# Performance work log

Hardware: AMD Instinct MI355X
Metric: run time of the kernel (lower is better)

## Reference

```python
import jax, jax.numpy as jnp
import numpy as np

B, N, DIM, NL, E = 8, 4096, 128, 3, 524288
NN = B * N


def setup_inputs() -> dict:
    key = jax.random.key(0)
    kx, ke, kw = jax.random.split(key, 3)
    x = jax.random.normal(kx, (B, N, DIM), dtype=jnp.float32)
    batch_edge_index = jax.random.randint(ke, (2, E), 0, NN, dtype=jnp.int32)
    wks = jax.random.split(kw, NL)
    Ws = jnp.stack([jax.random.normal(k, (DIM, DIM), dtype=jnp.float32) / np.sqrt(DIM)
                    for k in wks])  # [NL, DIM, DIM]
    bs = jnp.zeros((NL, DIM), dtype=jnp.float32)
    return {"x": x, "batch_edge_index": batch_edge_index, "Ws": Ws, "bs": bs}


def _gcn_layer(x, W, b, row, col, deg_inv_sqrt, n):
    # PyG GCNConv: h = x @ W; symmetric normalization over edges+self-loops;
    # scatter-add messages at targets (col); add bias.
    h = x @ W  # [n, DIM]
    norm = deg_inv_sqrt[row] * deg_inv_sqrt[col]  # [E+n]
    msg = h[row] * norm[:, None]  # gather at sources, scale
    return jax.ops.segment_sum(msg, col, num_segments=n) + b


def reference(x, batch_edge_index, Ws, bs):
    nb, npts, d = x.shape
    n = nb * npts
    h = x.reshape(n, d)
    # add self-loops once (same edge structure for all layers)
    loops = jnp.arange(n, dtype=batch_edge_index.dtype)
    row = jnp.concatenate([batch_edge_index[0], loops])
    col = jnp.concatenate([batch_edge_index[1], loops])
    deg = jax.ops.segment_sum(jnp.ones_like(col, dtype=h.dtype), col, num_segments=n)
    deg_inv_sqrt = jnp.where(deg > 0, jax.lax.rsqrt(jnp.maximum(deg, 1e-12)), 0.0)
    for i in range(NL):
        out = _gcn_layer(h, Ws[i], bs[i], row, col, deg_inv_sqrt, n)
        h = jax.nn.relu(h + out)  # residual + relu (dropout = identity in eval)
    return h.reshape(nb, npts, d)
```

## Files before the change

### kernel.cpp

```cpp
#include <hip/hip_runtime.h>


typedef __attribute__((ext_vector_type(8))) short short8;
typedef __attribute__((ext_vector_type(4))) float f32x4;
typedef __attribute__((ext_vector_type(2))) float f32x2;

__device__ inline ushort f2bf(float f) {
    union { float f; unsigned u; } v; v.f = f;
    unsigned u = v.u;
    return (ushort)((u + 0x7fffu + ((u >> 16) & 1u)) >> 16);
}
__device__ inline float2 bf2f(unsigned u) {
    union { unsigned i; float f; } a, b;
    a.i = u << 16;
    b.i = u & 0xffff0000u;
    return make_float2(a.f, b.f);
}
__device__ inline short8 pack8(f32x4 a, f32x4 b) {
    short8 r = { (short)f2bf(a.x), (short)f2bf(a.y), (short)f2bf(a.z), (short)f2bf(a.w),
                 (short)f2bf(b.x), (short)f2bf(b.y), (short)f2bf(b.z), (short)f2bf(b.w) };
    return r;
}
__device__ inline unsigned char f2fp8(float f) {
    return (unsigned char)(__builtin_amdgcn_cvt_pk_fp8_f32(f, f, 0, false) & 0xff);
}
__device__ inline float2 fp8x2(ushort v) {
    f32x2 lo = __builtin_amdgcn_cvt_pk_f32_fp8((int)v, false);
    return make_float2(lo.x, lo.y);
}

__global__ __launch_bounds__(256) void k_scan1(const int* __restrict__ deg,
                                               int* __restrict__ offs,
                                               int* __restrict__ bsum, int n) {
    __shared__ int sm[256];
    int t = threadIdx.x, i = blockIdx.x * 256 + t;
    int v = (i < n) ? deg[i] : 0;
    sm[t] = v;
    __syncthreads();
    for (int off = 1; off < 256; off <<= 1) {
        int u = (t >= off) ? sm[t - off] : 0;
        __syncthreads();
        sm[t] += u;
        __syncthreads();
    }
    if (i < n) offs[i] = sm[t] - v;
    if (t == 255) bsum[blockIdx.x] = sm[255];
}

__global__ __launch_bounds__(256) void k_scan3(int* __restrict__ offs,
                                               const int* __restrict__ bsum,
                                               const int* __restrict__ deg,
                                               int* __restrict__ cnt,
                                               float* __restrict__ dis,
                                               unsigned* __restrict__ g32,
                                               int n, int E) {
    __shared__ int red[256];
    int t = threadIdx.x, bid = blockIdx.x;
    red[t] = (t < 128 && t < bid) ? bsum[t] : 0;
    __syncthreads();
    for (int off = 128; off >= 1; off >>= 1) {
        if (t < off) red[t] += red[t + off];
        __syncthreads();
    }
    int base = red[0];
    int i = bid * 256 + t;
    if (i < n) {
        int o = offs[i] + base;
        offs[i] = o;
        cnt[i] = o;
        dis[i] = rsqrtf((float)(deg[i] + 1));
    }
    if (i == 0) offs[n] = E;
    if (i < 32) g32[(size_t)n * 32 + i] = 0;
}

__global__ void k_csr(const int* __restrict__ row, const int* __restrict__ col,
                      int* __restrict__ cnt, ushort* __restrict__ csru, int E) {
    int i = blockIdx.x * blockDim.x + threadIdx.x;
    if (i < E) {
        int c = col[i];
        int p = atomicAdd(&cnt[c], 1);
        csru[p] = (ushort)row[i];
    }
}

#define GEMM_BODY(A0, A1, A2, A3)                                               \
    f32x4 acc[8] = {};                                                          \
    _Pragma("unroll")                                                           \
    for (int nf = 0; nf < 8; ++nf) {                                            \
        const unsigned* wr = &Wl[nf * 16 + c][0];                               \
        int sx = (c & 7) << 2;                                                  \
        int b = q * 4;                                                          \
        short8 b0 = *(const short8*)(wr + ((b +  0) ^ sx));                     \
        short8 b1 = *(const short8*)(wr + ((b + 16) ^ sx));                     \
        short8 b2 = *(const short8*)(wr + ((b + 32) ^ sx));                     \
        short8 b3 = *(const short8*)(wr + ((b + 48) ^ sx));                     \
        acc[nf] = __builtin_amdgcn_mfma_f32_16x16x32_bf16(A0, b0, acc[nf], 0, 0, 0); \
        acc[nf] = __builtin_amdgcn_mfma_f32_16x16x32_bf16(A1, b1, acc[nf], 0, 0, 0); \
        acc[nf] = __builtin_amdgcn_mfma_f32_16x16x32_bf16(A2, b2, acc[nf], 0, 0, 0); \
        acc[nf] = __builtin_amdgcn_mfma_f32_16x16x32_bf16(A3, b3, acc[nf], 0, 0, 0); \
    }                                                                           \
    _Pragma("unroll")                                                           \
    for (int nf = 0; nf < 8; ++nf) {                                            \
        int gc = nf * 16 + c;                                                   \
        g[(size_t)(rb + q * 4 + 0) * 128 + gc] = f2fp8(acc[nf][0]);             \
        g[(size_t)(rb + q * 4 + 1) * 128 + gc] = f2fp8(acc[nf][1]);             \
        g[(size_t)(rb + q * 4 + 2) * 128 + gc] = f2fp8(acc[nf][2]);             \
        g[(size_t)(rb + q * 4 + 3) * 128 + gc] = f2fp8(acc[nf][3]);             \
    }

#define W_STAGE(TILE)                                                            \
    __shared__ unsigned Wl[128][64];                                             \
    int tid = threadIdx.x;                                                       \
    {                                                                            \
        int nn = tid & 127, hf = tid >> 7;                                       \
        for (int qq = 0; qq < 32; ++qq) {                                        \
            int k2 = hf * 32 + qq;                                               \
            float lo = W[(size_t)(2 * k2) * 128 + nn];                           \
            float hi = W[(size_t)(2 * k2 + 1) * 128 + nn];                       \
            Wl[nn][k2 ^ ((nn & 7) << 2)] = ((unsigned)f2bf(hi) << 16) | f2bf(lo);\
        }                                                                        \
    }                                                                            \
    __syncthreads();                                                             \
    int w = tid >> 6, l = tid & 63;                                              \
    int rb = (TILE) * 64 + w * 16;                                               \
    int c = l & 15, q = l >> 4;

__global__ __launch_bounds__(256) void k_gemm(const unsigned* __restrict__ hb,
                                              const float* __restrict__ W,
                                              unsigned char* __restrict__ g, int n) {
    W_STAGE(blockIdx.x)
    const short8* arow = (const short8*)(hb + (size_t)(rb + c) * 64);
    short8 a0 = arow[q], a1 = arow[4 + q], a2 = arow[8 + q], a3 = arow[12 + q];
    GEMM_BODY(a0, a1, a2, a3)
}

__global__ __launch_bounds__(256) void k_l0(const float* __restrict__ x,
                                            const float* __restrict__ W,
                                            unsigned char* __restrict__ g,
                                            const int* __restrict__ col,
                                            int* __restrict__ deg,
                                            int n, int E) {
    int gtiles = n >> 6;
    if ((int)blockIdx.x >= gtiles) {
        int i = ((int)blockIdx.x - gtiles) * 256 + threadIdx.x;
        if (i < E) atomicAdd(&deg[col[i]], 1);
        return;
    }
    W_STAGE((int)blockIdx.x)
    const f32x4* xr = (const f32x4*)(x + (size_t)(rb + c) * 128);
    short8 a0 = pack8(xr[q * 2 +  0], xr[q * 2 +  1]);
    short8 a1 = pack8(xr[q * 2 +  8], xr[q * 2 +  9]);
    short8 a2 = pack8(xr[q * 2 + 16], xr[q * 2 + 17]);
    short8 a3 = pack8(xr[q * 2 + 24], xr[q * 2 + 25]);
    GEMM_BODY(a0, a1, a2, a3)
}

__global__ __launch_bounds__(256) void k_gather(const ushort* __restrict__ g,
                                                unsigned* __restrict__ hb,
                                                const float* __restrict__ dis,
                                                const float* __restrict__ bias,
                                                const int* __restrict__ offs,
                                                const ushort* __restrict__ csru,
                                                const float* __restrict__ xres,
                                                float* __restrict__ outp,
                                                int n, int use_x, int last) {
    int wid = threadIdx.x >> 6, lane = threadIdx.x & 63;
    int node = blockIdx.x * 4 + wid;
    if (node >= n) return;

    float dn = dis[node];
    float2 acc;
    {
        float2 f = fp8x2(g[(size_t)node * 64 + lane]);
        acc.x = f.x * dn; acc.y = f.y * dn;
    }
    int s = offs[node];
    int deg = offs[node + 1] - s;
    for (int j0 = 0; j0 < deg; j0 += 64) {
        int rem = deg - j0;
        int m = rem < 64 ? rem : 64;
        int idx = n; float dsl = 0.f;
        if (lane < m) {
            idx = (int)__builtin_nontemporal_load(&csru[s + j0 + lane]);
            dsl = dis[idx];
        }
        int mc = (m + 15) & ~15;
        for (int t = 0; t < mc; t += 16) {
            ushort v[16];
#pragma unroll
            for (int u = 0; u < 16; ++u) {
                int r = __shfl(idx, t + u, 64);
                v[u] = g[(size_t)r * 64 + lane];
            }
            float ds[16];
#pragma unroll
            for (int u = 0; u < 16; ++u) ds[u] = __shfl(dsl, t + u, 64);
#pragma unroll
            for (int u = 0; u < 16; ++u) {
                float2 f = fp8x2(v[u]);
                acc.x = fmaf(f.x, ds[u], acc.x);
                acc.y = fmaf(f.y, ds[u], acc.y);
            }
        }
    }

    float2 bv = ((const float2*)bias)[lane];
    float2 hv;
    if (use_x) {
        hv = ((const float2*)xres)[(size_t)node * 64 + lane];
    } else {
        hv = bf2f(hb[(size_t)node * 64 + lane]);
    }
    float ox = fmaxf(hv.x + acc.x * dn + bv.x, 0.f);
    float oy = fmaxf(hv.y + acc.y * dn + bv.y, 0.f);
    if (last) {
        f32x2 o = { ox, oy };
        __builtin_nontemporal_store(o, (f32x2*)&outp[(size_t)node * 128 + lane * 2]);
    } else {
        hb[(size_t)node * 64 + lane] = ((unsigned)f2bf(oy) << 16) | f2bf(ox);
    }
}

static inline size_t al256(size_t x) { return (x + 255) & ~(size_t)255; }

extern "C" void kernel_launch(void* const* d_in, const int* in_sizes, int n_in,
                              void* d_out, int out_size, void* d_ws, size_t ws_size,
                              hipStream_t stream) {
    const float* x  = (const float*)d_in[0];
    const int*   ei = (const int*)d_in[1];
    const float* Ws = (const float*)d_in[2];
    const float* bs = (const float*)d_in[3];
    int n  = in_sizes[0] / 128;
    int E  = in_sizes[1] / 2;
    int NL = in_sizes[2] / (128 * 128);
    const int* rowp = ei;
    const int* colp = ei + E;

    char* ws = (char*)d_ws;
    size_t gplane  = al256((size_t)(n + 1) * 128);
    size_t hplane  = al256((size_t)(n + 1) * 256);
    unsigned char* g  = (unsigned char*)ws;
    unsigned*      hb = (unsigned*)(ws + gplane);
    char* p = ws + gplane + hplane;
    float* dis  = (float*)p;               p += al256((size_t)n * 4);
    int*   deg  = (int*)p;                 p += al256((size_t)n * 4);
    int*   offs = (int*)p;                 p += al256((size_t)(n + 1) * 4);
    int*   cnt  = (int*)p;                 p += al256((size_t)n * 4);
    int*   bsum = (int*)p;                 p += 512;
    ushort* csru = (ushort*)p;

    int nb = (n + 255) / 256;
    int gtiles = n / 64;
    int eblocks = (E + 255) / 256;

    (void)hipMemsetAsync(deg, 0, (size_t)n * 4, stream);
    k_l0<<<gtiles + eblocks, 256, 0, stream>>>(x, Ws, g, colp, deg, n, E);
    k_scan1<<<nb, 256, 0, stream>>>(deg, offs, bsum, n);
    k_scan3<<<nb, 256, 0, stream>>>(offs, bsum, deg, cnt, dis, (unsigned*)g, n, E);
    k_csr<<<eblocks, 256, 0, stream>>>(rowp, colp, cnt, csru, E);

    for (int l = 0; l < NL; ++l) {
        int last = (l + 1 == NL);
        if (l > 0)
            k_gemm<<<gtiles, 256, 0, stream>>>(hb, Ws + (size_t)l * 128 * 128,
                                               g, n);
        k_gather<<<(n + 3) / 4, 256, 0, stream>>>((const ushort*)g, hb, dis,
                                                  bs + (size_t)l * 128,
                                                  offs, csru, x,
                                                  (float*)d_out, n,
                                                  l == 0, last);
    }
}
```

Before: 150.3 us.

## Prescale GEMM output by source norm and gather two nodes per wavefront

Moves the per-source degree normalization out of the gather and into the producer: the GEMM epilogue multiplies each row by dis before the fp8 store, and k_scan3 rescales layer-0 rows in place. The gather then needs no per-edge dis lookup or shuffle and reduces to pure fp8 sums. Each half-wave handles one node with 4-byte loads (4 fp8 values per lane), so one wavefront covers two nodes. Tree-style partial sums replace the serial FMAs. The trade-off is an extra fp8 quantization after scaling, plus an extra read-modify-write pass over g in k_scan3.

```diff
diff --git a/kernel.cpp b/kernel.cpp
--- a/kernel.cpp
+++ b/kernel.cpp
@@ -4,6 +4,7 @@
 typedef __attribute__((ext_vector_type(8))) short short8;
 typedef __attribute__((ext_vector_type(4))) float f32x4;
 typedef __attribute__((ext_vector_type(2))) float f32x2;
+typedef __attribute__((ext_vector_type(2))) unsigned u32x2;
 
 __device__ inline ushort f2bf(float f) {
     union { float f; unsigned u; } v; v.f = f;
@@ -16,6 +17,11 @@
     b.i = u & 0xffff0000u;
     return make_float2(a.f, b.f);
 }
+__device__ inline f32x4 bf4(u32x2 v) {
+    float2 a = bf2f(v.x), b = bf2f(v.y);
+    f32x4 r = { a.x, a.y, b.x, b.y };
+    return r;
+}
 __device__ inline short8 pack8(f32x4 a, f32x4 b) {
     short8 r = { (short)f2bf(a.x), (short)f2bf(a.y), (short)f2bf(a.z), (short)f2bf(a.w),
                  (short)f2bf(b.x), (short)f2bf(b.y), (short)f2bf(b.z), (short)f2bf(b.w) };
@@ -24,9 +30,16 @@
 __device__ inline unsigned char f2fp8(float f) {
     return (unsigned char)(__builtin_amdgcn_cvt_pk_fp8_f32(f, f, 0, false) & 0xff);
 }
-__device__ inline float2 fp8x2(ushort v) {
+__device__ inline unsigned pack4fp8(f32x4 v) {
+    unsigned u = (unsigned)__builtin_amdgcn_cvt_pk_fp8_f32(v.x, v.y, 0, false);
+    u = (unsigned)__builtin_amdgcn_cvt_pk_fp8_f32(v.z, v.w, (int)u, true);
+    return u;
+}
+__device__ inline f32x4 fp8x4(unsigned v) {
     f32x2 lo = __builtin_amdgcn_cvt_pk_f32_fp8((int)v, false);
-    return make_float2(lo.x, lo.y);
+    f32x2 hi = __builtin_amdgcn_cvt_pk_f32_fp8((int)v, true);
+    f32x4 r = { lo.x, lo.y, hi.x, hi.y };
+    return r;
 }
 
 __global__ __launch_bounds__(256) void k_scan1(const int* __restrict__ deg,
@@ -64,14 +77,28 @@
     }
     int base = red[0];
     int i = bid * 256 + t;
+    float dv = 0.f;
     if (i < n) {
         int o = offs[i] + base;
         offs[i] = o;
         cnt[i] = o;
-        dis[i] = rsqrtf((float)(deg[i] + 1));
+        dv = rsqrtf((float)(deg[i] + 1));
+        dis[i] = dv;
     }
     if (i == 0) offs[n] = E;
     if (i < 32) g32[(size_t)n * 32 + i] = 0;
+
+    int lane = t & 63;
+    int wbase = bid * 256 + (t & ~63);
+    int hl = lane & 31, sel = lane >> 5;
+    for (int rr = 0; rr < 64; rr += 2) {
+        int row = wbase + rr + sel;
+        float d = __shfl(dv, rr + sel, 64);
+        if (row < n) {
+            unsigned u = g32[(size_t)row * 32 + hl];
+            g32[(size_t)row * 32 + hl] = pack4fp8(fp8x4(u) * d);
+        }
+    }
 }
 
 __global__ void k_csr(const int* __restrict__ row, const int* __restrict__ col,
@@ -84,7 +111,7 @@
     }
 }
 
-#define GEMM_BODY(A0, A1, A2, A3)                                               \
+#define GEMM_MAIN(A0, A1, A2, A3)                                               \
     f32x4 acc[8] = {};                                                          \
     _Pragma("unroll")                                                           \
     for (int nf = 0; nf < 8; ++nf) {                                            \
@@ -99,14 +126,16 @@
         acc[nf] = __builtin_amdgcn_mfma_f32_16x16x32_bf16(A1, b1, acc[nf], 0, 0, 0); \
         acc[nf] = __builtin_amdgcn_mfma_f32_16x16x32_bf16(A2, b2, acc[nf], 0, 0, 0); \
         acc[nf] = __builtin_amdgcn_mfma_f32_16x16x32_bf16(A3, b3, acc[nf], 0, 0, 0); \
-    }                                                                           \
+    }
+
+#define GEMM_STORE(D0, D1, D2, D3)                                              \
     _Pragma("unroll")                                                           \
     for (int nf = 0; nf < 8; ++nf) {                                            \
         int gc = nf * 16 + c;                                                   \
-        g[(size_t)(rb + q * 4 + 0) * 128 + gc] = f2fp8(acc[nf][0]);             \
-        g[(size_t)(rb + q * 4 + 1) * 128 + gc] = f2fp8(acc[nf][1]);             \
-        g[(size_t)(rb + q * 4 + 2) * 128 + gc] = f2fp8(acc[nf][2]);             \
-        g[(size_t)(rb + q * 4 + 3) * 128 + gc] = f2fp8(acc[nf][3]);             \
+        g[(size_t)(rb + q * 4 + 0) * 128 + gc] = f2fp8(acc[nf][0] * (D0));      \
+        g[(size_t)(rb + q * 4 + 1) * 128 + gc] = f2fp8(acc[nf][1] * (D1));      \
+        g[(size_t)(rb + q * 4 + 2) * 128 + gc] = f2fp8(acc[nf][2] * (D2));      \
+        g[(size_t)(rb + q * 4 + 3) * 128 + gc] = f2fp8(acc[nf][3] * (D3));      \
     }
 
 #define W_STAGE(TILE)                                                            \
@@ -128,11 +157,15 @@
 
 __global__ __launch_bounds__(256) void k_gemm(const unsigned* __restrict__ hb,
                                               const float* __restrict__ W,
+                                              const float* __restrict__ dis,
                                               unsigned char* __restrict__ g, int n) {
     W_STAGE(blockIdx.x)
     const short8* arow = (const short8*)(hb + (size_t)(rb + c) * 64);
     short8 a0 = arow[q], a1 = arow[4 + q], a2 = arow[8 + q], a3 = arow[12 + q];
-    GEMM_BODY(a0, a1, a2, a3)
+    GEMM_MAIN(a0, a1, a2, a3)
+    float d0 = dis[rb + q * 4 + 0], d1 = dis[rb + q * 4 + 1];
+    float d2 = dis[rb + q * 4 + 2], d3 = dis[rb + q * 4 + 3];
+    GEMM_STORE(d0, d1, d2, d3)
 }
 
 __global__ __launch_bounds__(256) void k_l0(const float* __restrict__ x,
@@ -153,10 +186,11 @@
     short8 a1 = pack8(xr[q * 2 +  8], xr[q * 2 +  9]);
     short8 a2 = pack8(xr[q * 2 + 16], xr[q * 2 + 17]);
     short8 a3 = pack8(xr[q * 2 + 24], xr[q * 2 + 25]);
-    GEMM_BODY(a0, a1, a2, a3)
-}
-
-__global__ __launch_bounds__(256) void k_gather(const ushort* __restrict__ g,
+    GEMM_MAIN(a0, a1, a2, a3)
+    GEMM_STORE(1.f, 1.f, 1.f, 1.f)
+}
+
+__global__ __launch_bounds__(256) void k_gather(const unsigned* __restrict__ g32,
                                                 unsigned* __restrict__ hb,
                                                 const float* __restrict__ dis,
                                                 const float* __restrict__ bias,
@@ -166,59 +200,51 @@
                                                 float* __restrict__ outp,
                                                 int n, int use_x, int last) {
     int wid = threadIdx.x >> 6, lane = threadIdx.x & 63;
-    int node = blockIdx.x * 4 + wid;
+    int sel = lane >> 5, hl = lane & 31;
+    int node = blockIdx.x * 8 + wid * 2 + sel;
     if (node >= n) return;
 
-    float dn = dis[node];
-    float2 acc;
-    {
-        float2 f = fp8x2(g[(size_t)node * 64 + lane]);
-        acc.x = f.x * dn; acc.y = f.y * dn;
-    }
+    f32x4 acc = fp8x4(g32[(size_t)node * 32 + hl]);
     int s = offs[node];
     int deg = offs[node + 1] - s;
-    for (int j0 = 0; j0 < deg; j0 += 64) {
+    for (int j0 = 0; j0 < deg; j0 += 32) {
         int rem = deg - j0;
-        int m = rem < 64 ? rem : 64;
-        int idx = n; float dsl = 0.f;
-        if (lane < m) {
-            idx = (int)__builtin_nontemporal_load(&csru[s + j0 + lane]);
-            dsl = dis[idx];
-        }
+        int m = rem < 32 ? rem : 32;
+        int idx = (hl < m) ? (int)__builtin_nontemporal_load(&csru[s + j0 + hl]) : n;
         int mc = (m + 15) & ~15;
         for (int t = 0; t < mc; t += 16) {
-            ushort v[16];
+            unsigned v[16];
 #pragma unroll
             for (int u = 0; u < 16; ++u) {
-                int r = __shfl(idx, t + u, 64);
-                v[u] = g[(size_t)r * 64 + lane];
+                int r = __shfl(idx, t + u, 32);
+                v[u] = g32[(size_t)r * 32 + hl];
             }
-            float ds[16];
-#pragma unroll
-            for (int u = 0; u < 16; ++u) ds[u] = __shfl(dsl, t + u, 64);
-#pragma unroll
-            for (int u = 0; u < 16; ++u) {
-                float2 f = fp8x2(v[u]);
-                acc.x = fmaf(f.x, ds[u], acc.x);
-                acc.y = fmaf(f.y, ds[u], acc.y);
-            }
+            f32x4 s0 = (fp8x4(v[0]) + fp8x4(v[1])) + (fp8x4(v[2]) + fp8x4(v[3]));
+            f32x4 s1 = (fp8x4(v[4]) + fp8x4(v[5])) + (fp8x4(v[6]) + fp8x4(v[7]));
+            f32x4 s2 = (fp8x4(v[8]) + fp8x4(v[9])) + (fp8x4(v[10]) + fp8x4(v[11]));
+            f32x4 s3 = (fp8x4(v[12]) + fp8x4(v[13])) + (fp8x4(v[14]) + fp8x4(v[15]));
+            acc += (s0 + s1) + (s2 + s3);
         }
     }
-
-    float2 bv = ((const float2*)bias)[lane];
-    float2 hv;
+    float dn = dis[node];
+    f32x4 bv = ((const f32x4*)bias)[hl];
+    f32x4 hv;
     if (use_x) {
-        hv = ((const float2*)xres)[(size_t)node * 64 + lane];
+        hv = __builtin_nontemporal_load(&((const f32x4*)xres)[(size_t)node * 32 + hl]);
     } else {
-        hv = bf2f(hb[(size_t)node * 64 + lane]);
-    }
-    float ox = fmaxf(hv.x + acc.x * dn + bv.x, 0.f);
-    float oy = fmaxf(hv.y + acc.y * dn + bv.y, 0.f);
+        u32x2 h2 = __builtin_nontemporal_load(&((const u32x2*)hb)[(size_t)node * 32 + hl]);
+        hv = bf4(h2);
+    }
+    f32x4 o = acc * dn + hv + bv;
+    o.x = fmaxf(o.x, 0.f); o.y = fmaxf(o.y, 0.f);
+    o.z = fmaxf(o.z, 0.f); o.w = fmaxf(o.w, 0.f);
     if (last) {
-        f32x2 o = { ox, oy };
-        __builtin_nontemporal_store(o, (f32x2*)&outp[(size_t)node * 128 + lane * 2]);
+        __builtin_nontemporal_store(o, &((f32x4*)outp)[(size_t)node * 32 + hl]);
     } else {
-        hb[(size_t)node * 64 + lane] = ((unsigned)f2bf(oy) << 16) | f2bf(ox);
+        u32x2 pk;
+        pk.x = ((unsigned)f2bf(o.y) << 16) | f2bf(o.x);
+        pk.y = ((unsigned)f2bf(o.w) << 16) | f2bf(o.z);
+        __builtin_nontemporal_store(pk, &((u32x2*)hb)[(size_t)node * 32 + hl]);
     }
 }
 
@@ -264,8 +290,8 @@
         int last = (l + 1 == NL);
         if (l > 0)
             k_gemm<<<gtiles, 256, 0, stream>>>(hb, Ws + (size_t)l * 128 * 128,
-                                               g, n);
-        k_gather<<<(n + 3) / 4, 256, 0, stream>>>((const ushort*)g, hb, dis,
+                                               dis, g, n);
+        k_gather<<<(n + 7) / 8, 256, 0, stream>>>((const unsigned*)g, hb, dis,
                                                   bs + (size_t)l * 128,
                                                   offs, csru, x,
                                                   (float*)d_out, n,
```

Result: faster. 142.3 us (-5.3%).
